# Performance work log

Hardware: AMD Instinct MI355X
Metric: run time of the kernel (lower is better)

## Reference

```python
import jax, jax.numpy as jnp
import numpy as np

B, V, F, P = 32, 256, 128, 64

def setup_inputs() -> dict:
    key = jax.random.key(0)
    k1, k2, k3, k4, k5 = jax.random.split(key, 5)
    q2_obs_scaled = jax.random.uniform(k1, (B, P), dtype=jnp.float32) * 3.0
    amplitude_logits = jax.random.normal(k2, (B, 1, F, P), dtype=jnp.float32)
    volumes = jax.random.uniform(k3, (V, 1), dtype=jnp.float32) + 0.5  # NonNeg, ~median 1
    filters = jax.random.uniform(k4, (1, F), dtype=jnp.float32) * 3.0  # NonNeg q2 positions
    sigma = jax.random.uniform(k5, (), dtype=jnp.float32) * 0.025 + 0.015  # in [0.015, 0.04]
    return {"q2_obs_scaled": q2_obs_scaled, "amplitude_logits": amplitude_logits,
            "volumes": volumes, "filters": filters, "sigma": sigma}

def reference(q2_obs_scaled, amplitude_logits, volumes, filters, sigma):
    # q2_filters: (V,1)*(1,F) -> (V,F) -> (1,V,F,1)
    q2_filters = (volumes * filters)[None, :, :, None]
    # q2_obs_scaled: (B,P) -> (B,1,1,P); difference: (B,V,F,P)
    difference = q2_filters - q2_obs_scaled[:, None, None, :]
    amplitudes = jax.nn.softmax(amplitude_logits, axis=3)  # (B,1,F,P)
    inv = 1.0 / (sigma + 0.001)
    distances = amplitudes * jnp.exp(-0.5 * (difference * inv) ** 2)
    metric = jnp.sum(distances, axis=3)  # (B,V,F)
    return metric
```

## Files before the change

kernel.cpp:

```cpp
#include <hip/hip_runtime.h>

#define B 32
#define V 256
#define F 128
#define P 64
#define VT 8

#define LOG2E 1.44269504088896340736f

__global__ __launch_bounds__(256) void extraction_kernel(
    const float* __restrict__ q2,
    const float* __restrict__ logits,
    const float* __restrict__ vol,
    const float* __restrict__ filt,
    const float* __restrict__ sigma_p,
    float* __restrict__ out)
{
    const int bid = blockIdx.x;
    const int b   = bid >> 5;
    const int v0  = (bid & 31) * VT;
    const int tid = threadIdx.x;
    const int f   = tid & (F - 1);
    const int vh  = tid >> 7;

    float amp[P];
    const float4* lg4 = (const float4*)(logits + (b * F + f) * P);
    float m = -3.0e38f;
    #pragma unroll
    for (int j = 0; j < P / 4; ++j) {
        float4 t = lg4[j];
        amp[4 * j + 0] = t.x;
        amp[4 * j + 1] = t.y;
        amp[4 * j + 2] = t.z;
        amp[4 * j + 3] = t.w;
        m = fmaxf(m, fmaxf(fmaxf(t.x, t.y), fmaxf(t.z, t.w)));
    }
    float sum = 0.f;
    #pragma unroll
    for (int p = 0; p < P; ++p) {
        float e = __builtin_amdgcn_exp2f((amp[p] - m) * LOG2E);
        amp[p] = e;
        sum += e;
    }
    const float rs = 1.0f / sum;
    #pragma unroll
    for (int p = 0; p < P; ++p) amp[p] *= rs;

    const float sig = sigma_p[0];
    const float inv = 1.0f / (sig + 0.001f);
    const float s = sqrtf(0.5f * LOG2E) * inv;

    float qs[P];
    #pragma unroll
    for (int p = 0; p < P; ++p)
        qs[p] = __uint_as_float(
            __builtin_amdgcn_readfirstlane(__float_as_uint(q2[b * P + p])));

    const float ff = filt[f];

    #pragma unroll 1
    for (int k = 0; k < VT / 2; ++k) {
        const int v = v0 + 2 * k + vh;
        const float x = vol[v] * ff;
        float a0 = 0.f, a1 = 0.f, a2 = 0.f, a3 = 0.f;
        #pragma unroll
        for (int p = 0; p < P; p += 4) {
            float t0 = (qs[p + 0] - x) * s;
            float t1 = (qs[p + 1] - x) * s;
            float t2 = (qs[p + 2] - x) * s;
            float t3 = (qs[p + 3] - x) * s;
            a0 += amp[p + 0] * __builtin_amdgcn_exp2f(-(t0 * t0));
            a1 += amp[p + 1] * __builtin_amdgcn_exp2f(-(t1 * t1));
            a2 += amp[p + 2] * __builtin_amdgcn_exp2f(-(t2 * t2));
            a3 += amp[p + 3] * __builtin_amdgcn_exp2f(-(t3 * t3));
        }
        out[(b * V + v) * F + f] = (a0 + a1) + (a2 + a3);
    }
}

extern "C" void kernel_launch(void* const* d_in, const int* in_sizes, int n_in,
                              void* d_out, int out_size, void* d_ws, size_t ws_size,
                              hipStream_t stream) {
    const float* q2     = (const float*)d_in[0];
    const float* logits = (const float*)d_in[1];
    const float* vol    = (const float*)d_in[2];
    const float* filt   = (const float*)d_in[3];
    const float* sigma  = (const float*)d_in[4];
    float* out = (float*)d_out;

    extraction_kernel<<<B * (V / VT), 256, 0, stream>>>(q2, logits, vol, filt, sigma, out);
}
```

Baseline: 78.61 us.

## Precompute softmax in separate kernel and fold sigma scale into inputs

```diff
diff --git a/kernel.cpp b/kernel.cpp
--- a/kernel.cpp
+++ b/kernel.cpp
@@ -8,9 +8,30 @@
 
 #define LOG2E 1.44269504088896340736f
 
+__global__ __launch_bounds__(256) void softmax_kernel(
+    const float* __restrict__ logits,
+    float* __restrict__ amp_ws)
+{
+    const int row  = blockIdx.x * 4 + (threadIdx.x >> 6);
+    const int lane = threadIdx.x & 63;
+    const int idx  = row * P + lane;
+
+    float l = logits[idx];
+    float m = l;
+    #pragma unroll
+    for (int off = 32; off > 0; off >>= 1)
+        m = fmaxf(m, __shfl_xor(m, off, 64));
+    float e = __builtin_amdgcn_exp2f((l - m) * LOG2E);
+    float s = e;
+    #pragma unroll
+    for (int off = 32; off > 0; off >>= 1)
+        s += __shfl_xor(s, off, 64);
+    amp_ws[idx] = e / s;
+}
+
 __global__ __launch_bounds__(256) void extraction_kernel(
     const float* __restrict__ q2,
-    const float* __restrict__ logits,
+    const float* __restrict__ amp_ws,
     const float* __restrict__ vol,
     const float* __restrict__ filt,
     const float* __restrict__ sigma_p,
@@ -23,52 +44,40 @@
     const int f   = tid & (F - 1);
     const int vh  = tid >> 7;
 
+    const float sig = sigma_p[0];
+    const float inv = 1.0f / (sig + 0.001f);
+    const float scl = sqrtf(0.5f * LOG2E) * inv;
+
     float amp[P];
-    const float4* lg4 = (const float4*)(logits + (b * F + f) * P);
-    float m = -3.0e38f;
+    const float4* a4 = (const float4*)(amp_ws + (b * F + f) * P);
     #pragma unroll
     for (int j = 0; j < P / 4; ++j) {
-        float4 t = lg4[j];
+        float4 t = a4[j];
         amp[4 * j + 0] = t.x;
         amp[4 * j + 1] = t.y;
         amp[4 * j + 2] = t.z;
         amp[4 * j + 3] = t.w;
-        m = fmaxf(m, fmaxf(fmaxf(t.x, t.y), fmaxf(t.z, t.w)));
     }
-    float sum = 0.f;
-    #pragma unroll
-    for (int p = 0; p < P; ++p) {
-        float e = __builtin_amdgcn_exp2f((amp[p] - m) * LOG2E);
-        amp[p] = e;
-        sum += e;
-    }
-    const float rs = 1.0f / sum;
-    #pragma unroll
-    for (int p = 0; p < P; ++p) amp[p] *= rs;
-
-    const float sig = sigma_p[0];
-    const float inv = 1.0f / (sig + 0.001f);
-    const float s = sqrtf(0.5f * LOG2E) * inv;
 
     float qs[P];
     #pragma unroll
     for (int p = 0; p < P; ++p)
-        qs[p] = __uint_as_float(
-            __builtin_amdgcn_readfirstlane(__float_as_uint(q2[b * P + p])));
+        qs[p] = __uint_as_float(__builtin_amdgcn_readfirstlane(
+                    __float_as_uint(q2[b * P + p] * scl)));
 
-    const float ff = filt[f];
+    const float ffs = filt[f] * scl;
 
     #pragma unroll 1
     for (int k = 0; k < VT / 2; ++k) {
         const int v = v0 + 2 * k + vh;
-        const float x = vol[v] * ff;
+        const float x = vol[v] * ffs;
         float a0 = 0.f, a1 = 0.f, a2 = 0.f, a3 = 0.f;
         #pragma unroll
         for (int p = 0; p < P; p += 4) {
-            float t0 = (qs[p + 0] - x) * s;
-            float t1 = (qs[p + 1] - x) * s;
-            float t2 = (qs[p + 2] - x) * s;
-            float t3 = (qs[p + 3] - x) * s;
+            float t0 = qs[p + 0] - x;
+            float t1 = qs[p + 1] - x;
+            float t2 = qs[p + 2] - x;
+            float t3 = qs[p + 3] - x;
             a0 += amp[p + 0] * __builtin_amdgcn_exp2f(-(t0 * t0));
             a1 += amp[p + 1] * __builtin_amdgcn_exp2f(-(t1 * t1));
             a2 += amp[p + 2] * __builtin_amdgcn_exp2f(-(t2 * t2));
@@ -87,6 +96,8 @@
     const float* filt   = (const float*)d_in[3];
     const float* sigma  = (const float*)d_in[4];
     float* out = (float*)d_out;
+    float* amp_ws = (float*)d_ws;
 
-    extraction_kernel<<<B * (V / VT), 256, 0, stream>>>(q2, logits, vol, filt, sigma, out);
+    softmax_kernel<<<B * F / 4, 256, 0, stream>>>(logits, amp_ws);
+    extraction_kernel<<<B * (V / VT), 256, 0, stream>>>(q2, amp_ws, vol, filt, sigma, out);
 }
```

After: 80.70 us. 2.7% more time.
